# Optimization experiments

Measured on AMD Instinct MI355X. Metric: run time of the kernel, lower is better.

The kernel has to match this reference:

```python
import jax, jax.numpy as jnp
import numpy as np

WINDOW = 33  # must match init_kwargs window_size (odd)


def setup_inputs() -> dict:
    key = jax.random.key(0)
    kq, kk, kv, km = jax.random.split(key, 4)
    B, S, D = 4, 2048, 256
    query = jax.random.normal(kq, (B, S, D), dtype=jnp.float32)
    k = jax.random.normal(kk, (B, S, D), dtype=jnp.float32)
    value = jax.random.normal(kv, (B, S, D), dtype=jnp.float32)
    mask = jax.random.randint(km, (B, S), 0, 2).astype(jnp.int32)
    return {"query": query, "key": k, "value": value, "mask": mask}


def reference(query, key, value, mask):
    # Local (sliding-window) attention, window centered at each position.
    B, S, D = query.shape
    half = WINDOW // 2
    offs = jnp.arange(-half, half + 1)                 # [W]
    idx = jnp.arange(S)[:, None] + offs[None, :]       # [S, W]
    valid = (idx >= 0) & (idx < S)                     # in-bounds window entries
    idxc = jnp.clip(idx, 0, S - 1)
    k_win = key[:, idxc]                               # [B, S, W, D]
    v_win = value[:, idxc]                             # [B, S, W, D]
    scores = jnp.einsum('bsd,bswd->bsw', query, k_win) / jnp.sqrt(jnp.float32(D))
    m_win = (mask[:, idxc] != 0) & valid[None]         # [B, S, W]
    scores = jnp.where(m_win, scores, jnp.float32(-1e10))  # masked_fill(-1e10)
    p_attn = jax.nn.softmax(scores, axis=-1)           # [B, S, W]
    values = jnp.einsum('bsw,bswd->bsd', p_attn, v_win)
    return values, p_attn
```

## Files before the change

kernel.cpp:

```cpp
#include <hip/hip_runtime.h>
#include <math.h>

#define S_LEN 2048
#define D_DIM 256
#define WIN 33
#define HALF 16
#define PT_STRIDE 72

typedef __attribute__((ext_vector_type(8))) short short8_t;
typedef __attribute__((ext_vector_type(4))) float f32x4;

__device__ inline unsigned short f32_to_bf16(float f) {
    unsigned u = __float_as_uint(f);
    return (unsigned short)((u + 0x7fffu + ((u >> 16) & 1u)) >> 16);
}

__device__ inline unsigned pack2_bf16(float lo, float hi) {
    unsigned a = __float_as_uint(lo) + 0x8000u;
    unsigned b = __float_as_uint(hi) + 0x8000u;
    return __builtin_amdgcn_perm(b, a, 0x07060302);
}

__device__ inline short8_t pack_bf16x8(float4 x, float4 y) {
    union { unsigned u[4]; short8_t s; } r;
    r.u[0] = pack2_bf16(x.x, x.y);
    r.u[1] = pack2_bf16(x.z, x.w);
    r.u[2] = pack2_bf16(y.x, y.y);
    r.u[3] = pack2_bf16(y.z, y.w);
    return r.s;
}

__global__ __launch_bounds__(128) void local_attn_wv(
    const float* __restrict__ q,
    const float* __restrict__ k,
    const float* __restrict__ v,
    const int*   __restrict__ mask,
    float* __restrict__ out_v,
    float* __restrict__ out_p)
{
    __shared__ __align__(16) unsigned short Pt[16 * PT_STRIDE];

    const int t    = threadIdx.x;
    const int lane = t & 63;
    const int h    = t >> 6;
    const int l15  = lane & 15;
    const int q4   = lane >> 4;

    const int bid  = blockIdx.x;
    const int tile = ((bid & 7) << 6) | (bid >> 3);
    const int b    = tile >> 7;
    const int s0   = (tile & 127) << 4;

    const float* qb = q + ((size_t)b * S_LEN + s0) * D_DIM;
    const float* kb = k + (size_t)b * S_LEN * D_DIM;
    const float* vb = v + (size_t)b * S_LEN * D_DIM;

    if (h == 0) {
        int  krow[3]; bool mv[3];
#pragma unroll
        for (int ct = 0; ct < 3; ++ct) {
            const int kv    = s0 - HALF + ct * 16 + l15;
            const bool valid = (kv >= 0) && (kv < S_LEN);
            const int kc    = min(max(kv, 0), S_LEN - 1);
            krow[ct] = kc;
            mv[ct]   = valid && (mask[b * S_LEN + kc] != 0);
        }
        short8_t aq[8];
#pragma unroll
        for (int ks = 0; ks < 8; ++ks) {
            const float* p = qb + l15 * D_DIM + ks * 32 + q4 * 8;
            const float4 x = *(const float4*)p;
            const float4 y = *(const float4*)(p + 4);
            aq[ks] = pack_bf16x8(x, y);
        }
        f32x4 acc[3];
        acc[0] = (f32x4){0.f,0.f,0.f,0.f};
        acc[1] = (f32x4){0.f,0.f,0.f,0.f};
        acc[2] = (f32x4){0.f,0.f,0.f,0.f};
#pragma unroll
        for (int ct = 0; ct < 3; ++ct) {
            const float* kr = kb + (size_t)krow[ct] * D_DIM;
#pragma unroll
            for (int ks = 0; ks < 8; ++ks) {
                const float* p = kr + ks * 32 + q4 * 8;
                const float4 x = *(const float4*)p;
                const float4 y = *(const float4*)(p + 4);
                const short8_t bk = pack_bf16x8(x, y);
                acc[ct] = __builtin_amdgcn_mfma_f32_16x16x32_bf16(aq[ks], bk, acc[ct], 0, 0, 0);
            }
        }
        float sv[3][4];
#pragma unroll
        for (int ct = 0; ct < 3; ++ct)
#pragma unroll
            for (int r = 0; r < 4; ++r) {
                const int m = q4 * 4 + r;
                const int c = ct * 16 + l15;
                const int j = c - m;
                const bool inband = (j >= 0) && (j < WIN);
                const float s = acc[ct][r] * 0.0625f;
                sv[ct][r] = inband ? (mv[ct] ? s : -1e10f) : -1e30f;
            }
        float rmax[4], rinv[4];
#pragma unroll
        for (int r = 0; r < 4; ++r) {
            float m = fmaxf(fmaxf(sv[0][r], sv[1][r]), sv[2][r]);
            m = fmaxf(m, __shfl_xor(m, 1, 64));
            m = fmaxf(m, __shfl_xor(m, 2, 64));
            m = fmaxf(m, __shfl_xor(m, 4, 64));
            m = fmaxf(m, __shfl_xor(m, 8, 64));
            rmax[r] = m;
        }
#pragma unroll
        for (int ct = 0; ct < 3; ++ct)
#pragma unroll
            for (int r = 0; r < 4; ++r)
                sv[ct][r] = __expf(sv[ct][r] - rmax[r]);
#pragma unroll
        for (int r = 0; r < 4; ++r) {
            float s = sv[0][r] + sv[1][r] + sv[2][r];
            s += __shfl_xor(s, 1, 64);
            s += __shfl_xor(s, 2, 64);
            s += __shfl_xor(s, 4, 64);
            s += __shfl_xor(s, 8, 64);
            rinv[r] = 1.0f / s;
        }
#pragma unroll
        for (int ct = 0; ct < 3; ++ct)
#pragma unroll
            for (int r = 0; r < 4; ++r) {
                const int m = q4 * 4 + r;
                const int c = ct * 16 + l15;
                const float p = sv[ct][r] * rinv[r];
                Pt[m * PT_STRIDE + c] = f32_to_bf16(p);
                const int j = c - m;
                if (j >= 0 && j < WIN)
                    out_p[((size_t)(b * S_LEN + s0 + m)) * WIN + j] = p;
            }
#pragma unroll
        for (int r = 0; r < 4; ++r)
            Pt[(q4 * 4 + r) * PT_STRIDE + 48 + l15] = 0;
    }

    short8_t bv[8][2];
    {
        const float* vrk0[8];
        const float* vrk1[8];
#pragma unroll
        for (int j = 0; j < 8; ++j) {
            const int g0 = q4 * 8 + j;
            const int g1 = 32 + q4 * 8 + j;
            const int kv0 = min(max(s0 - HALF + g0, 0), S_LEN - 1);
            const int kv1 = min(max(s0 - HALF + g1, 0), S_LEN - 1);
            vrk0[j] = vb + (size_t)kv0 * D_DIM + h * 128;
            vrk1[j] = vb + (size_t)kv1 * D_DIM + h * 128;
        }
        const bool act1 = (q4 < 2);
        const short8_t zfrag = {0,0,0,0,0,0,0,0};
#pragma unroll
        for (int nt = 0; nt < 8; ++nt) {
            const int d = nt * 16 + l15;
            float4 x, y;
            x.x = vrk0[0][d]; x.y = vrk0[1][d]; x.z = vrk0[2][d]; x.w = vrk0[3][d];
            y.x = vrk0[4][d]; y.y = vrk0[5][d]; y.z = vrk0[6][d]; y.w = vrk0[7][d];
            bv[nt][0] = pack_bf16x8(x, y);
            if (act1) {
                x.x = vrk1[0][d]; x.y = vrk1[1][d]; x.z = vrk1[2][d]; x.w = vrk1[3][d];
                y.x = vrk1[4][d]; y.y = vrk1[5][d]; y.z = vrk1[6][d]; y.w = vrk1[7][d];
                bv[nt][1] = pack_bf16x8(x, y);
            } else {
                bv[nt][1] = zfrag;
            }
        }
    }
    __syncthreads();

    short8_t ap[2];
    ap[0] = *(const short8_t*)&Pt[l15 * PT_STRIDE + q4 * 8];
    ap[1] = *(const short8_t*)&Pt[l15 * PT_STRIDE + 32 + q4 * 8];

    f32x4 acc[8];
#pragma unroll
    for (int nt = 0; nt < 8; ++nt) acc[nt] = (f32x4){0.f,0.f,0.f,0.f};
#pragma unroll
    for (int nt = 0; nt < 8; ++nt) {
        acc[nt] = __builtin_amdgcn_mfma_f32_16x16x32_bf16(ap[0], bv[nt][0], acc[nt], 0, 0, 0);
        acc[nt] = __builtin_amdgcn_mfma_f32_16x16x32_bf16(ap[1], bv[nt][1], acc[nt], 0, 0, 0);
    }
    float* ob = out_v + ((size_t)b * S_LEN + s0) * D_DIM + h * 128;
#pragma unroll
    for (int nt = 0; nt < 8; ++nt)
#pragma unroll
        for (int r = 0; r < 4; ++r)
            ob[(size_t)(q4 * 4 + r) * D_DIM + nt * 16 + l15] = acc[nt][r];
}

extern "C" void kernel_launch(void* const* d_in, const int* in_sizes, int n_in,
                              void* d_out, int out_size, void* d_ws, size_t ws_size,
                              hipStream_t stream) {
    const float* q    = (const float*)d_in[0];
    const float* k    = (const float*)d_in[1];
    const float* v    = (const float*)d_in[2];
    const int*   mask = (const int*)d_in[3];

    const int B = 4;
    float* out_v = (float*)d_out;
    float* out_p = (float*)d_out + (size_t)B * S_LEN * D_DIM;

    const int blocks = B * (S_LEN / 16);
    local_attn_wv<<<blocks, 128, 0, stream>>>(q, k, v, mask, out_v, out_p);
}
```

Measured before the change: 84.73 us.

## Restructure local attention to 4 waves with LDS-staged V and split softmax

The block grows from two to four waves. Three waves each compute one 16-column tile of QK^T, and the scores go to shared memory. Softmax is then spread across all 256 threads, and V is loaded with coalesced float4 reads, converted to bf16 and staged in LDS instead of the old strided per-element global gathers. Each wave computes 64 output columns of PV. The aim is to remove the serialized single-wave QK/softmax phase and the uncoalesced V loads, at the cost of more LDS traffic, an extra barrier and higher register and LDS use.

New measurement: 87.02 us. 1.03x slower.

```diff
diff --git a/kernel.cpp b/kernel.cpp
--- a/kernel.cpp
+++ b/kernel.cpp
@@ -1,10 +1,11 @@
 #include <hip/hip_runtime.h>
-#include <math.h>
 
 #define S_LEN 2048
 #define D_DIM 256
 #define WIN 33
 #define HALF 16
+#define VR_STRIDE 266
+#define SC_STRIDE 68
 #define PT_STRIDE 72
 
 typedef __attribute__((ext_vector_type(8))) short short8_t;
@@ -14,23 +15,19 @@
     unsigned u = __float_as_uint(f);
     return (unsigned short)((u + 0x7fffu + ((u >> 16) & 1u)) >> 16);
 }
-
 __device__ inline unsigned pack2_bf16(float lo, float hi) {
     unsigned a = __float_as_uint(lo) + 0x8000u;
     unsigned b = __float_as_uint(hi) + 0x8000u;
     return __builtin_amdgcn_perm(b, a, 0x07060302);
 }
-
 __device__ inline short8_t pack_bf16x8(float4 x, float4 y) {
     union { unsigned u[4]; short8_t s; } r;
-    r.u[0] = pack2_bf16(x.x, x.y);
-    r.u[1] = pack2_bf16(x.z, x.w);
-    r.u[2] = pack2_bf16(y.x, y.y);
-    r.u[3] = pack2_bf16(y.z, y.w);
+    r.u[0] = pack2_bf16(x.x, x.y); r.u[1] = pack2_bf16(x.z, x.w);
+    r.u[2] = pack2_bf16(y.x, y.y); r.u[3] = pack2_bf16(y.z, y.w);
     return r.s;
 }
 
-__global__ __launch_bounds__(128) void local_attn_wv(
+__global__ __launch_bounds__(256) void local_attn_v5(
     const float* __restrict__ q,
     const float* __restrict__ k,
     const float* __restrict__ v,
@@ -38,11 +35,14 @@
     float* __restrict__ out_v,
     float* __restrict__ out_p)
 {
+    __shared__ __align__(16) unsigned short Vr[48 * VR_STRIDE];
+    __shared__ __align__(16) float          Sc[16 * SC_STRIDE];
     __shared__ __align__(16) unsigned short Pt[16 * PT_STRIDE];
+    __shared__ int wm[64];
 
     const int t    = threadIdx.x;
     const int lane = t & 63;
-    const int h    = t >> 6;
+    const int w    = t >> 6;
     const int l15  = lane & 15;
     const int q4   = lane >> 4;
 
@@ -55,144 +55,119 @@
     const float* kb = k + (size_t)b * S_LEN * D_DIM;
     const float* vb = v + (size_t)b * S_LEN * D_DIM;
 
-    if (h == 0) {
-        int  krow[3]; bool mv[3];
+    float4 vreg[12];
 #pragma unroll
-        for (int ct = 0; ct < 3; ++ct) {
-            const int kv    = s0 - HALF + ct * 16 + l15;
-            const bool valid = (kv >= 0) && (kv < S_LEN);
-            const int kc    = min(max(kv, 0), S_LEN - 1);
-            krow[ct] = kc;
-            mv[ct]   = valid && (mask[b * S_LEN + kc] != 0);
-        }
-        short8_t aq[8];
+    for (int it = 0; it < 12; ++it) {
+        const int lin = it * 256 + t;
+        const int g   = lin >> 6;
+        const int c4  = lin & 63;
+        const int idx = min(max(s0 - HALF + g, 0), S_LEN - 1);
+        vreg[it] = *(const float4*)(vb + (size_t)idx * D_DIM + c4 * 4);
+    }
+    if (t < 64) {
+        const int idx = s0 - HALF + t;
+        wm[t] = (idx >= 0 && idx < S_LEN) ? (mask[b * S_LEN + idx] != 0) : 0;
+    }
+
+    if (w < 3) {
+        const int c    = 16 * w + l15;
+        const int kidx = min(max(s0 - HALF + c, 0), S_LEN - 1);
+        const float* kr = kb + (size_t)kidx * D_DIM;
+        const float* qr = qb + l15 * D_DIM;
+        f32x4 acc = (f32x4){0.f, 0.f, 0.f, 0.f};
 #pragma unroll
         for (int ks = 0; ks < 8; ++ks) {
-            const float* p = qb + l15 * D_DIM + ks * 32 + q4 * 8;
-            const float4 x = *(const float4*)p;
-            const float4 y = *(const float4*)(p + 4);
-            aq[ks] = pack_bf16x8(x, y);
-        }
-        f32x4 acc[3];
-        acc[0] = (f32x4){0.f,0.f,0.f,0.f};
-        acc[1] = (f32x4){0.f,0.f,0.f,0.f};
-        acc[2] = (f32x4){0.f,0.f,0.f,0.f};
-#pragma unroll
-        for (int ct = 0; ct < 3; ++ct) {
-            const float* kr = kb + (size_t)krow[ct] * D_DIM;
-#pragma unroll
-            for (int ks = 0; ks < 8; ++ks) {
-                const float* p = kr + ks * 32 + q4 * 8;
-                const float4 x = *(const float4*)p;
-                const float4 y = *(const float4*)(p + 4);
-                const short8_t bk = pack_bf16x8(x, y);
-                acc[ct] = __builtin_amdgcn_mfma_f32_16x16x32_bf16(aq[ks], bk, acc[ct], 0, 0, 0);
-            }
-        }
-        float sv[3][4];
-#pragma unroll
-        for (int ct = 0; ct < 3; ++ct)
-#pragma unroll
-            for (int r = 0; r < 4; ++r) {
-                const int m = q4 * 4 + r;
-                const int c = ct * 16 + l15;
-                const int j = c - m;
-                const bool inband = (j >= 0) && (j < WIN);
-                const float s = acc[ct][r] * 0.0625f;
-                sv[ct][r] = inband ? (mv[ct] ? s : -1e10f) : -1e30f;
-            }
-        float rmax[4], rinv[4];
-#pragma unroll
-        for (int r = 0; r < 4; ++r) {
-            float m = fmaxf(fmaxf(sv[0][r], sv[1][r]), sv[2][r]);
-            m = fmaxf(m, __shfl_xor(m, 1, 64));
-            m = fmaxf(m, __shfl_xor(m, 2, 64));
-            m = fmaxf(m, __shfl_xor(m, 4, 64));
-            m = fmaxf(m, __shfl_xor(m, 8, 64));
-            rmax[r] = m;
+            const float* pq = qr + ks * 32 + q4 * 8;
+            const float* pk = kr + ks * 32 + q4 * 8;
+            const short8_t aq = pack_bf16x8(*(const float4*)pq, *(const float4*)(pq + 4));
+            const short8_t bk = pack_bf16x8(*(const float4*)pk, *(const float4*)(pk + 4));
+            acc = __builtin_amdgcn_mfma_f32_16x16x32_bf16(aq, bk, acc, 0, 0, 0);
         }
 #pragma unroll
-        for (int ct = 0; ct < 3; ++ct)
-#pragma unroll
-            for (int r = 0; r < 4; ++r)
-                sv[ct][r] = __expf(sv[ct][r] - rmax[r]);
-#pragma unroll
-        for (int r = 0; r < 4; ++r) {
-            float s = sv[0][r] + sv[1][r] + sv[2][r];
-            s += __shfl_xor(s, 1, 64);
-            s += __shfl_xor(s, 2, 64);
-            s += __shfl_xor(s, 4, 64);
-            s += __shfl_xor(s, 8, 64);
-            rinv[r] = 1.0f / s;
-        }
-#pragma unroll
-        for (int ct = 0; ct < 3; ++ct)
-#pragma unroll
-            for (int r = 0; r < 4; ++r) {
-                const int m = q4 * 4 + r;
-                const int c = ct * 16 + l15;
-                const float p = sv[ct][r] * rinv[r];
-                Pt[m * PT_STRIDE + c] = f32_to_bf16(p);
-                const int j = c - m;
-                if (j >= 0 && j < WIN)
-                    out_p[((size_t)(b * S_LEN + s0 + m)) * WIN + j] = p;
-            }
-#pragma unroll
         for (int r = 0; r < 4; ++r)
-            Pt[(q4 * 4 + r) * PT_STRIDE + 48 + l15] = 0;
+            Sc[(q4 * 4 + r) * SC_STRIDE + c] = acc[r];
     }
 
-    short8_t bv[8][2];
+#pragma unroll
+    for (int it = 0; it < 12; ++it) {
+        const int lin = it * 256 + t;
+        const int g   = lin >> 6;
+        const int c4  = lin & 63;
+        const unsigned u0 = pack2_bf16(vreg[it].x, vreg[it].y);
+        const unsigned u1 = pack2_bf16(vreg[it].z, vreg[it].w);
+        *(unsigned*)&Vr[g * VR_STRIDE + c4 * 4]     = u0;
+        *(unsigned*)&Vr[g * VR_STRIDE + c4 * 4 + 2] = u1;
+    }
+    __syncthreads();
+
     {
-        const float* vrk0[8];
-        const float* vrk1[8];
+        const int row = t >> 4;
+        const int e   = t & 15;
+        float vs[4], ps[4];
+        if (e < 12) {
+            const float4 s4 = *(const float4*)&Sc[row * SC_STRIDE + 4 * e];
+            const float sarr[4] = {s4.x, s4.y, s4.z, s4.w};
 #pragma unroll
-        for (int j = 0; j < 8; ++j) {
-            const int g0 = q4 * 8 + j;
-            const int g1 = 32 + q4 * 8 + j;
-            const int kv0 = min(max(s0 - HALF + g0, 0), S_LEN - 1);
-            const int kv1 = min(max(s0 - HALF + g1, 0), S_LEN - 1);
-            vrk0[j] = vb + (size_t)kv0 * D_DIM + h * 128;
-            vrk1[j] = vb + (size_t)kv1 * D_DIM + h * 128;
+            for (int kq = 0; kq < 4; ++kq) {
+                const int c = 4 * e + kq, j = c - row;
+                const bool inb = (j >= 0) && (j < WIN);
+                vs[kq] = inb ? (wm[c] ? sarr[kq] * 0.0625f : -1e10f) : -1e30f;
+            }
+        } else {
+#pragma unroll
+            for (int kq = 0; kq < 4; ++kq) vs[kq] = -1e30f;
         }
-        const bool act1 = (q4 < 2);
-        const short8_t zfrag = {0,0,0,0,0,0,0,0};
+        float m = fmaxf(fmaxf(vs[0], vs[1]), fmaxf(vs[2], vs[3]));
+        m = fmaxf(m, __shfl_xor(m, 1, 64));
+        m = fmaxf(m, __shfl_xor(m, 2, 64));
+        m = fmaxf(m, __shfl_xor(m, 4, 64));
+        m = fmaxf(m, __shfl_xor(m, 8, 64));
+        float s = 0.f;
 #pragma unroll
-        for (int nt = 0; nt < 8; ++nt) {
-            const int d = nt * 16 + l15;
-            float4 x, y;
-            x.x = vrk0[0][d]; x.y = vrk0[1][d]; x.z = vrk0[2][d]; x.w = vrk0[3][d];
-            y.x = vrk0[4][d]; y.y = vrk0[5][d]; y.z = vrk0[6][d]; y.w = vrk0[7][d];
-            bv[nt][0] = pack_bf16x8(x, y);
-            if (act1) {
-                x.x = vrk1[0][d]; x.y = vrk1[1][d]; x.z = vrk1[2][d]; x.w = vrk1[3][d];
-                y.x = vrk1[4][d]; y.y = vrk1[5][d]; y.z = vrk1[6][d]; y.w = vrk1[7][d];
-                bv[nt][1] = pack_bf16x8(x, y);
-            } else {
-                bv[nt][1] = zfrag;
-            }
+        for (int kq = 0; kq < 4; ++kq) { vs[kq] = __expf(vs[kq] - m); s += vs[kq]; }
+        s += __shfl_xor(s, 1, 64);
+        s += __shfl_xor(s, 2, 64);
+        s += __shfl_xor(s, 4, 64);
+        s += __shfl_xor(s, 8, 64);
+        const float rinv = 1.0f / s;
+        union { unsigned short u[4]; uint2 d; } pw;
+#pragma unroll
+        for (int kq = 0; kq < 4; ++kq) {
+            ps[kq]   = vs[kq] * rinv;
+            pw.u[kq] = f32_to_bf16(ps[kq]);
+        }
+        *(uint2*)&Pt[row * PT_STRIDE + 4 * e] = pw.d;
+        float* prow = out_p + ((size_t)(b * S_LEN + s0 + row)) * WIN;
+#pragma unroll
+        for (int kq = 0; kq < 4; ++kq) {
+            const int j = 4 * e + kq - row;
+            if (j >= 0 && j < WIN) prow[j] = ps[kq];
         }
     }
     __syncthreads();
 
-    short8_t ap[2];
-    ap[0] = *(const short8_t*)&Pt[l15 * PT_STRIDE + q4 * 8];
-    ap[1] = *(const short8_t*)&Pt[l15 * PT_STRIDE + 32 + q4 * 8];
-
-    f32x4 acc[8];
+    const short8_t ap0 = *(const short8_t*)&Pt[l15 * PT_STRIDE + q4 * 8];
+    const short8_t ap1 = *(const short8_t*)&Pt[l15 * PT_STRIDE + 32 + q4 * 8];
+    float* ob = out_v + ((size_t)b * S_LEN + s0) * D_DIM;
 #pragma unroll
-    for (int nt = 0; nt < 8; ++nt) acc[nt] = (f32x4){0.f,0.f,0.f,0.f};
+    for (int nt = 0; nt < 4; ++nt) {
+        const int d = 64 * w + 16 * nt + l15;
+        short8_t b0, b1;
 #pragma unroll
-    for (int nt = 0; nt < 8; ++nt) {
-        acc[nt] = __builtin_amdgcn_mfma_f32_16x16x32_bf16(ap[0], bv[nt][0], acc[nt], 0, 0, 0);
-        acc[nt] = __builtin_amdgcn_mfma_f32_16x16x32_bf16(ap[1], bv[nt][1], acc[nt], 0, 0, 0);
-    }
-    float* ob = out_v + ((size_t)b * S_LEN + s0) * D_DIM + h * 128;
+        for (int j = 0; j < 8; ++j)
+            b0[j] = (short)Vr[(q4 * 8 + j) * VR_STRIDE + d];
 #pragma unroll
-    for (int nt = 0; nt < 8; ++nt)
+        for (int j = 0; j < 8; ++j) {
+            const int g = min(32 + q4 * 8 + j, 47);
+            b1[j] = (short)Vr[g * VR_STRIDE + d];
+        }
+        f32x4 acc = (f32x4){0.f, 0.f, 0.f, 0.f};
+        acc = __builtin_amdgcn_mfma_f32_16x16x32_bf16(ap0, b0, acc, 0, 0, 0);
+        acc = __builtin_amdgcn_mfma_f32_16x16x32_bf16(ap1, b1, acc, 0, 0, 0);
 #pragma unroll
         for (int r = 0; r < 4; ++r)
-            ob[(size_t)(q4 * 4 + r) * D_DIM + nt * 16 + l15] = acc[nt][r];
+            ob[(size_t)(q4 * 4 + r) * D_DIM + d] = acc[r];
+    }
 }
 
 extern "C" void kernel_launch(void* const* d_in, const int* in_sizes, int n_in,
@@ -208,5 +183,5 @@
     float* out_p = (float*)d_out + (size_t)B * S_LEN * D_DIM;
 
     const int blocks = B * (S_LEN / 16);
-    local_attn_wv<<<blocks, 128, 0, stream>>>(q, k, v, mask, out_v, out_p);
+    local_attn_v5<<<blocks, 256, 0, stream>>>(q, k, v, mask, out_v, out_p);
 }
```
